# Optimization experiments

Hardware: AMD Instinct MI355X
Metric: run time of the kernel (lower is better)

Reference implementation:

```python
import jax, jax.numpy as jnp
import numpy as np

HIDDEN = 256
INPUT = 1
OUTPUT = 1
BATCH = 64
SEQ = 2048


def setup_inputs() -> dict:
    key = jax.random.key(0)
    ks = jax.random.split(key, 8)
    s_ih = 1.0 / np.sqrt(HIDDEN)  # torch nn.LSTM init: U(-1/sqrt(H), 1/sqrt(H))
    x = jax.random.normal(ks[0], (BATCH, SEQ, INPUT), dtype=jnp.float32)
    W_ih = jax.random.uniform(ks[1], (4 * HIDDEN, INPUT), jnp.float32, -s_ih, s_ih)
    W_hh = jax.random.uniform(ks[2], (4 * HIDDEN, HIDDEN), jnp.float32, -s_ih, s_ih)
    b_ih = jax.random.uniform(ks[3], (4 * HIDDEN,), jnp.float32, -s_ih, s_ih)
    b_hh = jax.random.uniform(ks[4], (4 * HIDDEN,), jnp.float32, -s_ih, s_ih)
    W_fc = jax.random.uniform(ks[5], (OUTPUT, HIDDEN), jnp.float32, -s_ih, s_ih)
    b_fc = jax.random.uniform(ks[6], (OUTPUT,), jnp.float32, -s_ih, s_ih)
    return {"x": x, "W_ih": W_ih, "W_hh": W_hh, "b_ih": b_ih,
            "b_hh": b_hh, "W_fc": W_fc, "b_fc": b_fc}


def reference(x, W_ih, W_hh, b_ih, b_hh, W_fc, b_fc):
    B, T, _ = x.shape
    H = W_hh.shape[1]
    # precompute input contribution to all gates: [B,T,4H] (input_dim=1)
    gx = jnp.einsum('bti,gi->btg', x, W_ih) + b_ih + b_hh
    gx_t = jnp.transpose(gx, (1, 0, 2))  # [T,B,4H] for scan over time
    h0 = jnp.zeros((B, H), x.dtype)
    c0 = jnp.zeros((B, H), x.dtype)

    def step(carry, g_t):
        h, c = carry
        gates = g_t + h @ W_hh.T                 # [B,4H]
        i, f, g, o = jnp.split(gates, 4, axis=-1)  # torch gate order i,f,g,o
        i = jax.nn.sigmoid(i)
        f = jax.nn.sigmoid(f)
        g = jnp.tanh(g)
        o = jax.nn.sigmoid(o)
        c = f * c + i * g
        h = o * jnp.tanh(c)
        return (h, c), h

    (h_n, c_n), hs = jax.lax.scan(step, (h0, c0), gx_t)
    out = jnp.transpose(hs, (1, 0, 2))           # [B,T,H]
    y = out @ W_fc.T + b_fc                      # fused linear head [B,T,1]
    return (y, (h_n[None], c_n[None]))           # match torch (num_layers=1, B, H)
```

## Files before the change

kernel.cpp:

```cpp
#include <hip/hip_runtime.h>
#include <hip/hip_fp16.h>

#define SEQT 2048
#define HID  256
#define NB   64

typedef int   int32x4 __attribute__((ext_vector_type(4)));
typedef _Float16 h2  __attribute__((ext_vector_type(2)));

#define LOG2E 1.4426950408889634f
static __device__ __forceinline__ float sigf(float x) {
  return __builtin_amdgcn_rcpf(1.f + __builtin_amdgcn_exp2f(-LOG2E * x));
}
static __device__ __forceinline__ float tanhf_fast(float x) {
  float e = __builtin_amdgcn_exp2f(-2.f * LOG2E * fabsf(x));
  float r = (1.f - e) * __builtin_amdgcn_rcpf(1.f + e);
  return copysignf(r, x);
}
static __device__ __forceinline__ float max4(float4 f) {
  return fmaxf(fmaxf(fabsf(f.x), fabsf(f.y)), fmaxf(fabsf(f.z), fabsf(f.w)));
}

__global__ __attribute__((amdgpu_flat_work_group_size(512, 512),
                          amdgpu_waves_per_eu(2, 2)))
void lstm_main(
    const float* __restrict__ x, const float* __restrict__ Wih,
    const float* __restrict__ Whh, const float* __restrict__ bih,
    const float* __restrict__ bhh, float* __restrict__ out,
    unsigned* __restrict__ hist)
{
  __shared__ __align__(16) int           gatesL[1024];
  __shared__ __align__(16) unsigned char qring[16 * 256];
  __shared__ __align__(16) unsigned      f16r[16 * 128];
  __shared__ float xs[SEQT];
  __shared__ float redf[9];

  const int t    = threadIdx.x;
  const int b    = blockIdx.x;
  const int w    = t >> 6;
  const int lane = t & 63;
  const int ko   = lane >> 4;
  const int lm   = lane & 15;

  ((float4*)xs)[t] = ((const float4*)(x + (size_t)b * SEQT))[t];
  if (t < 64) ((unsigned*)qring)[15 * 64 + t] = 0u;

  float mx = 0.f;
#pragma unroll
  for (int r = 0; r < 8; ++r) {
    const float* rp = Whh + (size_t)(128 * w + 16 * r + lm) * HID + 16 * ko;
#pragma unroll
    for (int kt = 0; kt < 4; ++kt) {
      const float4* p = (const float4*)(rp + 64 * kt);
      mx = fmaxf(mx, fmaxf(fmaxf(max4(p[0]), max4(p[1])),
                           fmaxf(max4(p[2]), max4(p[3]))));
    }
  }
#pragma unroll
  for (int o = 32; o; o >>= 1) mx = fmaxf(mx, __shfl_xor(mx, o, 64));
  if (lane == 0) redf[w] = mx;
  __syncthreads();
  if (t == 0) {
    float m = redf[0];
#pragma unroll
    for (int i = 1; i < 8; ++i) m = fmaxf(m, redf[i]);
    redf[8] = m;
  }
  __syncthreads();
  const float s_w  = redf[8];
  const float winv = 127.f / s_w;
  const float S    = s_w / (127.f * 127.f);

  int32x4 af[8][4];
#pragma unroll
  for (int r = 0; r < 8; ++r) {
    const float* rp = Whh + (size_t)(128 * w + 16 * r + lm) * HID + 16 * ko;
#pragma unroll
    for (int kt = 0; kt < 4; ++kt) {
      const float4* p = (const float4*)(rp + 64 * kt);
      int32x4 v;
#pragma unroll
      for (int d = 0; d < 4; ++d) {
        float4 f = p[d];
        int q0 = (int)__builtin_rintf(f.x * winv);
        int q1 = (int)__builtin_rintf(f.y * winv);
        int q2 = (int)__builtin_rintf(f.z * winv);
        int q3 = (int)__builtin_rintf(f.w * winv);
        v[d] = (q0 & 255) | ((q1 & 255) << 8) | ((q2 & 255) << 16) | ((q3 & 255) << 24);
      }
      af[r][kt] = v;
    }
  }

  float b4[4] = {0, 0, 0, 0}, w4[4] = {0, 0, 0, 0};
  if (t < 256) {
#pragma unroll
    for (int q = 0; q < 4; ++q) {
      int row = q * 256 + t;
      b4[q] = bih[row] + bhh[row];
      w4[q] = Wih[row];
    }
  }
  __syncthreads();

  unsigned* histb = hist + (size_t)b * SEQT * 128;
  float c = 0.f, h = 0.f;
  const int32x4 z4 = {0, 0, 0, 0};

  for (int s = 0; s < SEQT; ++s) {
    const unsigned char* qs = qring + ((s + 15) & 15) * 256;
    int32x4 bf0 = *(const int32x4*)(qs + 16 * ko);
    int32x4 bf1 = *(const int32x4*)(qs + 64 + 16 * ko);
    int32x4 bf2 = *(const int32x4*)(qs + 128 + 16 * ko);
    int32x4 bf3 = *(const int32x4*)(qs + 192 + 16 * ko);
#pragma unroll
    for (int r = 0; r < 8; ++r) {
      int32x4 a = __builtin_amdgcn_mfma_i32_16x16x64_i8(af[r][0], bf0, z4, 0, 0, 0);
      a = __builtin_amdgcn_mfma_i32_16x16x64_i8(af[r][1], bf1, a, 0, 0, 0);
      a = __builtin_amdgcn_mfma_i32_16x16x64_i8(af[r][2], bf2, a, 0, 0, 0);
      a = __builtin_amdgcn_mfma_i32_16x16x64_i8(af[r][3], bf3, a, 0, 0, 0);
      if (lm == 0) *(int32x4*)(gatesL + 128 * w + 16 * r + 4 * ko) = a;
    }
    __syncthreads();

    if (t < 256) {
      float xv = xs[s];
      float a0 = __builtin_fmaf((float)gatesL[t],       S, __builtin_fmaf(w4[0], xv, b4[0]));
      float a1 = __builtin_fmaf((float)gatesL[256 + t], S, __builtin_fmaf(w4[1], xv, b4[1]));
      float a2 = __builtin_fmaf((float)gatesL[512 + t], S, __builtin_fmaf(w4[2], xv, b4[2]));
      float a3 = __builtin_fmaf((float)gatesL[768 + t], S, __builtin_fmaf(w4[3], xv, b4[3]));
      float I = sigf(a0), F = sigf(a1), G = tanhf_fast(a2), O = sigf(a3);
      c = F * c + I * G;
      h = O * tanhf_fast(c);
      ((_Float16*)f16r)[(s & 15) * 256 + t] = (_Float16)h;
      int q = (int)__builtin_rintf(h * 127.f);
      ((char*)qring)[(s & 15) * 256 + t] = (char)q;
    }
    __syncthreads();

    if ((s & 15) == 15) {
      uint4 v = *(const uint4*)(f16r + 4 * t);
      *(uint4*)(histb + (size_t)(s - 15) * 128 + 4 * t) = v;
    }
  }

  if (t < 256) {
    out[NB * SEQT + b * HID + t]            = h;
    out[NB * SEQT + NB * HID + b * HID + t] = c;
  }
}

__global__ __launch_bounds__(256) void lstm_head(
    const unsigned* __restrict__ hist, const float* __restrict__ Wfc,
    const float* __restrict__ bfc, float* __restrict__ y)
{
  int gw   = (blockIdx.x * 256 + threadIdx.x) >> 6;
  int lane = threadIdx.x & 63;
  uint2 hv = ((const uint2*)(hist + (size_t)gw * 128))[lane];
  float4 w = ((const float4*)Wfc)[lane];
  h2 p0 = __builtin_bit_cast(h2, hv.x);
  h2 p1 = __builtin_bit_cast(h2, hv.y);
  float s = (float)p0.x * w.x + (float)p0.y * w.y +
            (float)p1.x * w.z + (float)p1.y * w.w;
#pragma unroll
  for (int m = 32; m; m >>= 1) s += __shfl_xor(s, m, 64);
  if (lane == 0) y[gw] = s + bfc[0];
}

extern "C" void kernel_launch(void* const* d_in, const int* in_sizes, int n_in,
                              void* d_out, int out_size, void* d_ws, size_t ws_size,
                              hipStream_t stream)
{
  const float* x   = (const float*)d_in[0];
  const float* Wih = (const float*)d_in[1];
  const float* Whh = (const float*)d_in[2];
  const float* bih = (const float*)d_in[3];
  const float* bhh = (const float*)d_in[4];
  const float* Wfc = (const float*)d_in[5];
  const float* bfc = (const float*)d_in[6];
  float* out      = (float*)d_out;
  unsigned* hist  = (unsigned*)d_ws;

  (void)in_sizes; (void)n_in; (void)out_size; (void)ws_size;

  lstm_main<<<dim3(NB), dim3(512), 0, stream>>>(x, Wih, Whh, bih, bhh, out, hist);
  lstm_head<<<dim3((NB * SEQT) / 4), dim3(256), 0, stream>>>(hist, Wfc, bfc, out);
}
```

Measured before the change: 2.001 ms.

## Remap gate rows per wave so each wave computes its own cell updates, dropping one barrier

Reassigns W_hh rows so each wave's MFMA tiles hold all four gates (i,f,g,o) for its own 32 hidden units, letting lanes take their gate values straight from the accumulators instead of going through a shared gatesL buffer. This removes one __syncthreads per timestep and the LDS round trip for gate values, and all 512 threads now do the nonlinearity work (half redundantly). It also switches to per-row int8 quantisation scales for W_hh, which can improve accuracy, and interleaves the MFMA chains across 8 independent accumulators for more instruction-level parallelism. An extra barrier is added only on history-flush steps to guard against overwriting the ring.

```diff
diff --git a/kernel.cpp b/kernel.cpp
--- a/kernel.cpp
+++ b/kernel.cpp
@@ -5,8 +5,8 @@
 #define HID  256
 #define NB   64
 
-typedef int   int32x4 __attribute__((ext_vector_type(4)));
-typedef _Float16 h2  __attribute__((ext_vector_type(2)));
+typedef int int32x4 __attribute__((ext_vector_type(4)));
+typedef _Float16 h2 __attribute__((ext_vector_type(2)));
 
 #define LOG2E 1.4426950408889634f
 static __device__ __forceinline__ float sigf(float x) {
@@ -23,17 +23,15 @@
 
 __global__ __attribute__((amdgpu_flat_work_group_size(512, 512),
                           amdgpu_waves_per_eu(2, 2)))
-void lstm_main(
-    const float* __restrict__ x, const float* __restrict__ Wih,
-    const float* __restrict__ Whh, const float* __restrict__ bih,
-    const float* __restrict__ bhh, float* __restrict__ out,
-    unsigned* __restrict__ hist)
+void lstm_main(const float* __restrict__ x, const float* __restrict__ Wih,
+               const float* __restrict__ Whh, const float* __restrict__ bih,
+               const float* __restrict__ bhh, float* __restrict__ out,
+               unsigned* __restrict__ hist)
 {
-  __shared__ __align__(16) int           gatesL[1024];
   __shared__ __align__(16) unsigned char qring[16 * 256];
   __shared__ __align__(16) unsigned      f16r[16 * 128];
   __shared__ float xs[SEQT];
-  __shared__ float redf[9];
+  __shared__ float rowS[1024];
 
   const int t    = threadIdx.x;
   const int b    = blockIdx.x;
@@ -41,40 +39,30 @@
   const int lane = t & 63;
   const int ko   = lane >> 4;
   const int lm   = lane & 15;
+  const int su   = (lm >> 2) & 1;
+  const int ru   = lm & 3;
+  const int u    = 32 * w + 16 * su + 4 * ko + ru;
 
   ((float4*)xs)[t] = ((const float4*)(x + (size_t)b * SEQT))[t];
   if (t < 64) ((unsigned*)qring)[15 * 64 + t] = 0u;
 
-  float mx = 0.f;
+  int32x4 af[8][4];
 #pragma unroll
   for (int r = 0; r < 8; ++r) {
-    const float* rp = Whh + (size_t)(128 * w + 16 * r + lm) * HID + 16 * ko;
+    const int q = r >> 1, sh = r & 1;
+    const int row = q * 256 + 32 * w + 16 * sh + lm;
+    const float* rp = Whh + (size_t)row * HID + 16 * ko;
+    float mx = 1e-20f;
 #pragma unroll
     for (int kt = 0; kt < 4; ++kt) {
       const float4* p = (const float4*)(rp + 64 * kt);
       mx = fmaxf(mx, fmaxf(fmaxf(max4(p[0]), max4(p[1])),
                            fmaxf(max4(p[2]), max4(p[3]))));
     }
-  }
-#pragma unroll
-  for (int o = 32; o; o >>= 1) mx = fmaxf(mx, __shfl_xor(mx, o, 64));
-  if (lane == 0) redf[w] = mx;
-  __syncthreads();
-  if (t == 0) {
-    float m = redf[0];
-#pragma unroll
-    for (int i = 1; i < 8; ++i) m = fmaxf(m, redf[i]);
-    redf[8] = m;
-  }
-  __syncthreads();
-  const float s_w  = redf[8];
-  const float winv = 127.f / s_w;
-  const float S    = s_w / (127.f * 127.f);
-
-  int32x4 af[8][4];
-#pragma unroll
-  for (int r = 0; r < 8; ++r) {
-    const float* rp = Whh + (size_t)(128 * w + 16 * r + lm) * HID + 16 * ko;
+    mx = fmaxf(mx, __shfl_xor(mx, 16, 64));
+    mx = fmaxf(mx, __shfl_xor(mx, 32, 64));
+    const float winv = 127.f / mx;
+    if (ko == 0) rowS[row] = mx * (1.f / (127.f * 127.f));
 #pragma unroll
     for (int kt = 0; kt < 4; ++kt) {
       const float4* p = (const float4*)(rp + 64 * kt);
@@ -92,61 +80,76 @@
     }
   }
 
-  float b4[4] = {0, 0, 0, 0}, w4[4] = {0, 0, 0, 0};
-  if (t < 256) {
+  float biasu[4], wihu[4];
 #pragma unroll
-    for (int q = 0; q < 4; ++q) {
-      int row = q * 256 + t;
-      b4[q] = bih[row] + bhh[row];
-      w4[q] = Wih[row];
-    }
+  for (int q = 0; q < 4; ++q) {
+    int row = q * 256 + u;
+    biasu[q] = bih[row] + bhh[row];
+    wihu[q]  = Wih[row];
   }
   __syncthreads();
+  float Su[4];
+#pragma unroll
+  for (int q = 0; q < 4; ++q) Su[q] = rowS[q * 256 + u];
 
   unsigned* histb = hist + (size_t)b * SEQT * 128;
   float c = 0.f, h = 0.f;
   const int32x4 z4 = {0, 0, 0, 0};
 
   for (int s = 0; s < SEQT; ++s) {
+    float xv = xs[s];
     const unsigned char* qs = qring + ((s + 15) & 15) * 256;
-    int32x4 bf0 = *(const int32x4*)(qs + 16 * ko);
-    int32x4 bf1 = *(const int32x4*)(qs + 64 + 16 * ko);
-    int32x4 bf2 = *(const int32x4*)(qs + 128 + 16 * ko);
-    int32x4 bf3 = *(const int32x4*)(qs + 192 + 16 * ko);
+    int32x4 bf[4];
 #pragma unroll
-    for (int r = 0; r < 8; ++r) {
-      int32x4 a = __builtin_amdgcn_mfma_i32_16x16x64_i8(af[r][0], bf0, z4, 0, 0, 0);
-      a = __builtin_amdgcn_mfma_i32_16x16x64_i8(af[r][1], bf1, a, 0, 0, 0);
-      a = __builtin_amdgcn_mfma_i32_16x16x64_i8(af[r][2], bf2, a, 0, 0, 0);
-      a = __builtin_amdgcn_mfma_i32_16x16x64_i8(af[r][3], bf3, a, 0, 0, 0);
-      if (lm == 0) *(int32x4*)(gatesL + 128 * w + 16 * r + 4 * ko) = a;
+    for (int kt = 0; kt < 4; ++kt)
+      bf[kt] = *(const int32x4*)(qs + 64 * kt + 16 * ko);
+
+    int32x4 acc[8];
+#pragma unroll
+    for (int r = 0; r < 8; ++r)
+      acc[r] = __builtin_amdgcn_mfma_i32_16x16x64_i8(af[r][0], bf[0], z4, 0, 0, 0);
+#pragma unroll
+    for (int kt = 1; kt < 4; ++kt)
+#pragma unroll
+      for (int r = 0; r < 8; ++r)
+        acc[r] = __builtin_amdgcn_mfma_i32_16x16x64_i8(af[r][kt], bf[kt], acc[r], 0, 0, 0);
+
+    float aq[4];
+#pragma unroll
+    for (int q = 0; q < 4; ++q) {
+      int32x4 v0 = acc[2 * q], v1 = acc[2 * q + 1];
+      int e0 = su ? v1[0] : v0[0];
+      int e1 = su ? v1[1] : v0[1];
+      int e2 = su ? v1[2] : v0[2];
+      int e3 = su ? v1[3] : v0[3];
+      int g01 = (ru & 1) ? e1 : e0;
+      int g23 = (ru & 1) ? e3 : e2;
+      int gv  = (ru & 2) ? g23 : g01;
+      aq[q] = __builtin_fmaf((float)gv, Su[q],
+                             __builtin_fmaf(wihu[q], xv, biasu[q]));
     }
-    __syncthreads();
 
-    if (t < 256) {
-      float xv = xs[s];
-      float a0 = __builtin_fmaf((float)gatesL[t],       S, __builtin_fmaf(w4[0], xv, b4[0]));
-      float a1 = __builtin_fmaf((float)gatesL[256 + t], S, __builtin_fmaf(w4[1], xv, b4[1]));
-      float a2 = __builtin_fmaf((float)gatesL[512 + t], S, __builtin_fmaf(w4[2], xv, b4[2]));
-      float a3 = __builtin_fmaf((float)gatesL[768 + t], S, __builtin_fmaf(w4[3], xv, b4[3]));
-      float I = sigf(a0), F = sigf(a1), G = tanhf_fast(a2), O = sigf(a3);
-      c = F * c + I * G;
-      h = O * tanhf_fast(c);
-      ((_Float16*)f16r)[(s & 15) * 256 + t] = (_Float16)h;
-      int q = (int)__builtin_rintf(h * 127.f);
-      ((char*)qring)[(s & 15) * 256 + t] = (char)q;
+    float I = sigf(aq[0]), F = sigf(aq[1]), G = tanhf_fast(aq[2]), O = sigf(aq[3]);
+    c = F * c + I * G;
+    h = O * tanhf_fast(c);
+
+    if (lm < 8) {
+      int qv = (int)__builtin_rintf(h * 127.f);
+      ((char*)qring)[(s & 15) * 256 + u]      = (char)qv;
+      ((_Float16*)f16r)[(s & 15) * 256 + u]   = (_Float16)h;
     }
     __syncthreads();
 
     if ((s & 15) == 15) {
       uint4 v = *(const uint4*)(f16r + 4 * t);
       *(uint4*)(histb + (size_t)(s - 15) * 128 + 4 * t) = v;
+      __syncthreads();
     }
   }
 
-  if (t < 256) {
-    out[NB * SEQT + b * HID + t]            = h;
-    out[NB * SEQT + NB * HID + b * HID + t] = c;
+  if (lm < 8) {
+    out[NB * SEQT + b * HID + u]            = h;
+    out[NB * SEQT + NB * HID + b * HID + u] = c;
   }
 }
 
```

New measurement: 1.643 ms. 17.9% less time.
